# Optimization experiments

Measured on AMD Instinct MI355X. Metric: run time of the kernel, lower is better.

## Reference

```python
import jax, jax.numpy as jnp
import numpy as np

C = 256
NUM_HEADS = 4
GROUPS = 32  # max(1, 256//8), divides 256
EPS = 1e-5


def setup_inputs() -> dict:
    key = jax.random.key(0)
    ks = jax.random.split(key, 7)
    B, H, W = 4, 64, 64
    s = 0.02
    return {
        "x": jax.random.normal(ks[0], (B, C, H, W), dtype=jnp.float32),
        "norm_gamma": jnp.ones((C,), jnp.float32),
        "norm_beta": jnp.zeros((C,), jnp.float32),
        "qkv_w": jax.random.normal(ks[1], (3 * C, C), jnp.float32) * s,  # 1x1 conv kernel squeezed
        "qkv_b": jax.random.normal(ks[2], (3 * C,), jnp.float32) * s,
        "proj_w": jax.random.normal(ks[3], (C, C), jnp.float32) * s,
        "proj_b": jax.random.normal(ks[4], (C,), jnp.float32) * s,
    }


def reference(x, norm_gamma, norm_beta, qkv_w, qkv_b, proj_w, proj_b):
    B, Cc, H, W = x.shape
    hd = Cc // NUM_HEADS
    scale = hd ** -0.5

    # GroupNorm over (channels-per-group, H, W)
    xg = x.reshape(B, GROUPS, Cc // GROUPS, H, W)
    mu = xg.mean(axis=(2, 3, 4), keepdims=True)
    var = xg.var(axis=(2, 3, 4), keepdims=True)
    h = ((xg - mu) * jax.lax.rsqrt(var + EPS)).reshape(B, Cc, H, W)
    h = h * norm_gamma[:, None, None] + norm_beta[:, None, None]

    # 1x1 conv QKV: [B,3C,H,W]
    qkv = jnp.einsum('bchw,oc->bohw', h, qkv_w) + qkv_b[:, None, None]
    q, k, v = jnp.split(qkv, 3, axis=1)

    def heads(t):  # [B,C,H,W] -> [B,nh,HW,hd]
        return t.reshape(B, NUM_HEADS, hd, H * W).transpose(0, 1, 3, 2)

    q, k, v = heads(q), heads(k), heads(v)
    attn = jnp.einsum('bhnd,bhmd->bhnm', q, k) * scale  # [B,nh,HW,HW]
    attn = jax.nn.softmax(attn, axis=-1)
    out = jnp.einsum('bhnm,bhmd->bhnd', attn, v)  # [B,nh,HW,hd]
    out = out.transpose(0, 1, 3, 2).reshape(B, Cc, H, W)

    out = jnp.einsum('bchw,oc->bohw', out, proj_w) + proj_b[:, None, None]
    return x + out
```

## Files before the change

### kernel.cpp

```cpp
#include <hip/hip_runtime.h>
#include <hip/hip_bf16.h>
#include <stdint.h>

typedef unsigned short u16;
typedef __attribute__((ext_vector_type(8))) short bf16x8;
typedef __attribute__((ext_vector_type(4))) float f32x4;
typedef __attribute__((ext_vector_type(16))) float f32x16;

#define HW 4096
#define CC 256
#define QSCALE 0.18033688011112042f

__device__ __forceinline__ u16 f2bf(float f) {
    union { float f; uint32_t i; } v; v.f = f;
    uint32_t x = v.i;
    return (u16)((x + 0x7fffu + ((x >> 16) & 1u)) >> 16);
}

__device__ __forceinline__ float fast_exp2(float x) {
#if __has_builtin(__builtin_amdgcn_exp2f)
    return __builtin_amdgcn_exp2f(x);
#else
    return exp2f(x);
#endif
}

__device__ __forceinline__ unsigned cvt_pk_bf16(float lo, float hi) {
    unsigned r;
    asm("v_cvt_pk_bf16_f32 %0, %1, %2" : "=v"(r) : "v"(lo), "v"(hi));
    return r;
}

__device__ __forceinline__ void plane_swap(unsigned& a, unsigned& b) {
#if __has_builtin(__builtin_amdgcn_permlane32_swap)
    auto r = __builtin_amdgcn_permlane32_swap(a, b, false, false);
    a = r[0]; b = r[1];
#else
    unsigned ax = __shfl_xor((int)a, 32);
    unsigned bx = __shfl_xor((int)b, 32);
    bool hi = (threadIdx.x & 32) != 0;
    unsigned na = hi ? bx : a;
    unsigned nb = hi ? b : ax;
    a = na; b = nb;
#endif
}

#define MFMA16(a, b, c) __builtin_amdgcn_mfma_f32_16x16x32_bf16(a, b, c, 0, 0, 0)
#define MFMA32(a, b, c) __builtin_amdgcn_mfma_f32_32x32x16_bf16(a, b, c, 0, 0, 0)

__global__ void k_wsc(const float* __restrict__ qkv_w, const float* __restrict__ proj_w,
                      const float* __restrict__ x,
                      u16* __restrict__ wqkv, u16* __restrict__ wproj, float* __restrict__ stats) {
    int bid = blockIdx.x;
    if (bid < 1024) {
        int bg = bid >> 3, slab = bid & 7;
        const float4* p = reinterpret_cast<const float4*>(x + (size_t)bg * 32768 + slab * 4096);
        float s = 0.f, ss = 0.f;
        for (int i = 0; i < 4; ++i) {
            float4 v = p[threadIdx.x + i * 256];
            s += v.x + v.y + v.z + v.w;
            ss += v.x * v.x + v.y * v.y + v.z * v.z + v.w * v.w;
        }
        __shared__ float rs[256], rss[256];
        rs[threadIdx.x] = s; rss[threadIdx.x] = ss;
        __syncthreads();
        for (int off = 128; off > 0; off >>= 1) {
            if (threadIdx.x < off) { rs[threadIdx.x] += rs[threadIdx.x + off]; rss[threadIdx.x] += rss[threadIdx.x + off]; }
            __syncthreads();
        }
        if (threadIdx.x == 0) {
            stats[bid * 2] = rs[0];
            stats[bid * 2 + 1] = rss[0];
        }
    } else {
        int i = (bid - 1024) * 256 + threadIdx.x;
        if (i < 768 * 256) {
            int o = i >> 8;
            float sc = (o < 256) ? QSCALE : 1.0f;
            wqkv[i] = f2bf(qkv_w[i] * sc);
        }
        int j = i - 768 * 256;
        if (j >= 0 && j < 256 * 256) wproj[j] = f2bf(proj_w[j]);
    }
}

__global__ __launch_bounds__(256) void k_gnt(const float* __restrict__ x, const float* __restrict__ stats,
                                             const float* __restrict__ gamma, const float* __restrict__ beta,
                                             u16* __restrict__ h_t) {
    int bid = blockIdx.x;
    int b = bid >> 8;
    int cb = (bid >> 6) & 3;
    int nb = bid & 63;
    int t = threadIdx.x;
    int cl = t >> 2;
    int ch = t & 3;
    int c = cb * 64 + cl;
    int g = c >> 3;
    float sum = 0.f, ssum = 0.f;
    for (int s = 0; s < 8; ++s) {
        sum  += stats[((b * 32 + g) * 8 + s) * 2];
        ssum += stats[((b * 32 + g) * 8 + s) * 2 + 1];
    }
    float mu = sum * (1.f / 32768.f);
    float var = ssum * (1.f / 32768.f) - mu * mu;
    float rsg = rsqrtf(var + 1e-5f);
    float ga = gamma[c], be = beta[c];
    __shared__ float T[64][66];
    const float4* p = reinterpret_cast<const float4*>(x + ((size_t)(b * CC + c)) * HW + nb * 64 + ch * 16);
    for (int j = 0; j < 4; ++j) {
        float4 v = p[j];
        int nbase = ch * 16 + j * 4;
        T[nbase + 0][cl] = (v.x - mu) * rsg * ga + be;
        T[nbase + 1][cl] = (v.y - mu) * rsg * ga + be;
        T[nbase + 2][cl] = (v.z - mu) * rsg * ga + be;
        T[nbase + 3][cl] = (v.w - mu) * rsg * ga + be;
    }
    __syncthreads();
    int nl = t >> 2;
    union { u16 u[16]; uint4 q[2]; } pk;
    for (int j = 0; j < 16; ++j) pk.u[j] = f2bf(T[nl][ch * 16 + j]);
    u16* dst = h_t + ((size_t)b * HW + nb * 64 + nl) * CC + cb * 64 + ch * 16;
    *reinterpret_cast<uint4*>(dst) = pk.q[0];
    *reinterpret_cast<uint4*>(dst + 8) = pk.q[1];
}

__global__ __launch_bounds__(256) void k_qkv(const u16* __restrict__ wqkv, const u16* __restrict__ h_t,
                                             const float* __restrict__ qkv_b,
                                             u16* __restrict__ qk_t, u16* __restrict__ v_o) {
    int bid = blockIdx.x;
    int b = bid / 192;
    int rem = bid % 192;
    int om = rem >> 5;
    int nb = rem & 31;
    int o0 = om * 128, n0 = nb * 128;
    int t = threadIdx.x;
    int wid = t >> 6, lane = t & 63;
    int wm = wid >> 1, wn = wid & 1;
    int l15 = lane & 15, lg = lane >> 4;

    __shared__ u16 sA[128 * 40], sB[128 * 40];
    f32x4 acc[4][4];
    for (int i = 0; i < 4; ++i) for (int j = 0; j < 4; ++j) acc[i][j] = (f32x4)0.f;

    const u16* gA = wqkv + (size_t)o0 * 256;
    const u16* gB = h_t + ((size_t)b * HW + n0) * CC;
    int row = t >> 1, half = t & 1;

    for (int kt = 0; kt < 8; ++kt) {
        __syncthreads();
        {
            const uint4* pa = reinterpret_cast<const uint4*>(gA + (size_t)row * 256 + kt * 32 + half * 16);
            uint4 a0 = pa[0], a1 = pa[1];
            const uint4* pb = reinterpret_cast<const uint4*>(gB + (size_t)row * 256 + kt * 32 + half * 16);
            uint4 b0 = pb[0], b1 = pb[1];
            *reinterpret_cast<uint4*>(&sA[row * 40 + half * 16]) = a0;
            *reinterpret_cast<uint4*>(&sA[row * 40 + half * 16 + 8]) = a1;
            *reinterpret_cast<uint4*>(&sB[row * 40 + half * 16]) = b0;
            *reinterpret_cast<uint4*>(&sB[row * 40 + half * 16 + 8]) = b1;
        }
        __syncthreads();
        bf16x8 af[4], bfr[4];
        for (int mt = 0; mt < 4; ++mt)
            af[mt] = *reinterpret_cast<const bf16x8*>(&sA[(wm * 64 + mt * 16 + l15) * 40 + lg * 8]);
        for (int nt = 0; nt < 4; ++nt)
            bfr[nt] = *reinterpret_cast<const bf16x8*>(&sB[(wn * 64 + nt * 16 + l15) * 40 + lg * 8]);
        for (int mt = 0; mt < 4; ++mt)
            for (int nt = 0; nt < 4; ++nt)
                acc[mt][nt] = MFMA16(af[mt], bfr[nt], acc[mt][nt]);
    }

    if (o0 < 512) {
        for (int mt = 0; mt < 4; ++mt) {
            int ob = o0 + wm * 64 + mt * 16 + lg * 4;
            float bias[4];
            for (int r = 0; r < 4; ++r) {
                int o = ob + r;
                bias[r] = qkv_b[o] * (o < 256 ? QSCALE : 1.0f);
            }
            for (int nt = 0; nt < 4; ++nt) {
                int n = n0 + wn * 64 + nt * 16 + l15;
                union { u16 u[4]; uint2 q; } pk;
                for (int r = 0; r < 4; ++r) pk.u[r] = f2bf(acc[mt][nt][r] + bias[r]);
                *reinterpret_cast<uint2*>(qk_t + ((size_t)b * HW + n) * 512 + ob) = pk.q;
            }
        }
    } else {
        for (int mt = 0; mt < 4; ++mt) {
            int ob = o0 + wm * 64 + mt * 16 + lg * 4;
            for (int nt = 0; nt < 4; ++nt) {
                int n = n0 + wn * 64 + nt * 16 + l15;
                for (int r = 0; r < 4; ++r) {
                    int o = ob + r;
                    float bias = qkv_b[o];
                    v_o[((size_t)b * 256 + (o - 512)) * HW + n] = f2bf(acc[mt][nt][r] + bias);
                }
            }
        }
    }
}

__global__ __launch_bounds__(512, 4) void k_attn(const u16* __restrict__ qk_t, const u16* __restrict__ v_o,
                                                 u16* __restrict__ ao_t) {
    int bid = blockIdx.x;
    int swz = (bid & 7) * 64 + (bid >> 3);
    int qb = swz & 31, head = (swz >> 5) & 3, b = swz >> 7;
    int n0 = qb * 128;
    int t = threadIdx.x;
    int kg = t >> 8;
    int wq = (t >> 6) & 3;
    int lane = t & 63, l31 = lane & 31, h = lane >> 5;

    __shared__ u16 lds[2 * 2 * 2 * 64 * 72];

    const u16* qbase = qk_t + ((size_t)b * HW + n0 + wq * 32 + l31) * 512 + head * 64 + h * 8;
    bf16x8 qf[4];
#pragma unroll
    for (int cs = 0; cs < 4; ++cs) qf[cs] = *reinterpret_cast<const bf16x8*>(qbase + cs * 16);

    const u16* gK = qk_t + (size_t)b * HW * 512 + 256 + head * 64;
    const u16* gV = v_o + ((size_t)b * 256 + head * 64) * (size_t)HW;

    int tIn = t & 255;
    int srow = tIn >> 3, sch = tIn & 7;
    const u16* pk0 = gK + (size_t)(kg * 2048 + srow) * 512 + sch * 8;
    const u16* pk1 = pk0 + 32 * 512;
    const u16* pv0 = gV + (size_t)srow * HW + kg * 2048 + sch * 8;
    const u16* pv1 = pv0 + 32 * HW;
    uint4 rk0 = *reinterpret_cast<const uint4*>(pk0);
    uint4 rk1 = *reinterpret_cast<const uint4*>(pk1);
    uint4 rv0 = *reinterpret_cast<const uint4*>(pv0);
    uint4 rv1 = *reinterpret_cast<const uint4*>(pv1);

    f32x16 o0 = (f32x16)0.f, o1 = (f32x16)0.f;
    float l_run = 0.f;
    u16* gb = lds + kg * 18432;

    for (int ti = 0; ti < 32; ++ti) {
        u16* bK = gb + (ti & 1) * 9216;
        u16* bV = bK + 4608;
        *reinterpret_cast<uint4*>(bK + srow * 72 + sch * 8) = rk0;
        *reinterpret_cast<uint4*>(bK + (srow + 32) * 72 + sch * 8) = rk1;
        *reinterpret_cast<uint4*>(bV + srow * 72 + sch * 8) = rv0;
        *reinterpret_cast<uint4*>(bV + (srow + 32) * 72 + sch * 8) = rv1;
        __syncthreads();

        if (ti < 31) {
            pk0 += 64 * 512; pk1 += 64 * 512; pv0 += 64; pv1 += 64;
            rk0 = *reinterpret_cast<const uint4*>(pk0);
            rk1 = *reinterpret_cast<const uint4*>(pk1);
            rv0 = *reinterpret_cast<const uint4*>(pv0);
            rv1 = *reinterpret_cast<const uint4*>(pv1);
        }

        f32x16 s0 = (f32x16)0.f, s1 = (f32x16)0.f;
        __builtin_amdgcn_s_setprio(1);
#pragma unroll
        for (int cs = 0; cs < 4; ++cs) {
            bf16x8 k0 = *reinterpret_cast<const bf16x8*>(bK + l31 * 72 + cs * 16 + h * 8);
            bf16x8 k1 = *reinterpret_cast<const bf16x8*>(bK + (l31 + 32) * 72 + cs * 16 + h * 8);
            s0 = MFMA32(k0, qf[cs], s0);
            s1 = MFMA32(k1, qf[cs], s1);
        }
        __builtin_amdgcn_s_setprio(0);

        float ps = 0.f;
#pragma unroll
        for (int i = 0; i < 16; ++i) { float e = fast_exp2(s0[i]); s0[i] = e; ps += e; }
#pragma unroll
        for (int i = 0; i < 16; ++i) { float e = fast_exp2(s1[i]); s1[i] = e; ps += e; }
        l_run += ps;

        unsigned dws[2][8];
#pragma unroll
        for (int a = 0; a < 4; ++a) {
            dws[0][2 * a]     = cvt_pk_bf16(s0[4 * a],     s0[4 * a + 1]);
            dws[0][2 * a + 1] = cvt_pk_bf16(s0[4 * a + 2], s0[4 * a + 3]);
            dws[1][2 * a]     = cvt_pk_bf16(s1[4 * a],     s1[4 * a + 1]);
            dws[1][2 * a + 1] = cvt_pk_bf16(s1[4 * a + 2], s1[4 * a + 3]);
        }
        bf16x8 pf[4];
#pragma unroll
        for (int ks = 0; ks < 4; ++ks) {
            int kt = ks >> 1, sf = ks & 1;
            unsigned A0 = dws[kt][4 * sf + 0], B0 = dws[kt][4 * sf + 2];
            unsigned A1 = dws[kt][4 * sf + 1], B1 = dws[kt][4 * sf + 3];
            plane_swap(A0, B0);
            plane_swap(A1, B1);
            union { unsigned d[4]; bf16x8 v; } u;
            u.d[0] = A0; u.d[1] = A1; u.d[2] = B0; u.d[3] = B1;
            pf[ks] = u.v;
        }

        __builtin_amdgcn_s_setprio(1);
#pragma unroll
        for (int ks = 0; ks < 4; ++ks) {
            bf16x8 v0 = *reinterpret_cast<const bf16x8*>(bV + l31 * 72 + ks * 16 + h * 8);
            bf16x8 v1 = *reinterpret_cast<const bf16x8*>(bV + (l31 + 32) * 72 + ks * 16 + h * 8);
            o0 = MFMA32(v0, pf[ks], o0);
            o1 = MFMA32(v1, pf[ks], o1);
        }
        __builtin_amdgcn_s_setprio(0);
    }

    l_run += __shfl_xor(l_run, 32);

    float* Of = (float*)lds;
    float* Lf = (float*)lds + 8192;
    u16* E = lds + 18432;

    __syncthreads();
    if (kg == 1) {
#pragma unroll
        for (int i = 0; i < 16; ++i) {
            Of[wq * 2048 + i * 64 + lane] = o0[i];
            Of[wq * 2048 + (16 + i) * 64 + lane] = o1[i];
        }
        Lf[wq * 64 + lane] = l_run;
    }
    __syncthreads();
    if (kg == 0) {
#pragma unroll
        for (int i = 0; i < 16; ++i) {
            o0[i] += Of[wq * 2048 + i * 64 + lane];
            o1[i] += Of[wq * 2048 + (16 + i) * 64 + lane];
        }
        l_run += Lf[wq * 64 + lane];
        float inv = 1.0f / l_run;
        int qrow = wq * 32 + l31;
#pragma unroll
        for (int r = 0; r < 16; ++r) {
            int d = (r & 3) + 8 * (r >> 2) + 4 * h;
            E[qrow * 72 + d]      = f2bf(o0[r] * inv);
            E[qrow * 72 + 32 + d] = f2bf(o1[r] * inv);
        }
    }
    __syncthreads();
#pragma unroll
    for (int i = 0; i < 2; ++i) {
        int item = i * 512 + t;
        int row = item >> 3, cb = item & 7;
        uint4 w = *reinterpret_cast<const uint4*>(E + row * 72 + cb * 8);
        *reinterpret_cast<uint4*>(ao_t + ((size_t)b * HW + n0 + row) * 256 + head * 64 + cb * 8) = w;
    }
}

__global__ __launch_bounds__(256) void k_proj(const u16* __restrict__ wproj, const u16* __restrict__ ao_t,
                                              const float* __restrict__ proj_b, const float* __restrict__ x,
                                              float* __restrict__ out) {
    int bid = blockIdx.x;
    int b = bid >> 7;
    int om = (bid >> 6) & 1;
    int nb = bid & 63;
    int o0 = om * 128, n0 = nb * 64;
    int t = threadIdx.x;
    int wid = t >> 6, lane = t & 63;
    int wm = wid >> 1, wn = wid & 1;
    int l15 = lane & 15, lg = lane >> 4;

    __shared__ u16 sA[128 * 40], sB[64 * 40];
    f32x4 acc[4][2];
    for (int i = 0; i < 4; ++i) for (int j = 0; j < 2; ++j) acc[i][j] = (f32x4)0.f;

    const u16* gA = wproj + (size_t)o0 * 256;
    const u16* gB = ao_t + ((size_t)b * HW + n0) * CC;
    int rowA = t >> 1, halfA = t & 1;
    int rowB = t >> 2, qB = t & 3;

    for (int kt = 0; kt < 8; ++kt) {
        __syncthreads();
        {
            const uint4* pa = reinterpret_cast<const uint4*>(gA + (size_t)rowA * 256 + kt * 32 + halfA * 16);
            uint4 a0 = pa[0], a1 = pa[1];
            uint4 b0 = *reinterpret_cast<const uint4*>(gB + (size_t)rowB * 256 + kt * 32 + qB * 8);
            *reinterpret_cast<uint4*>(&sA[rowA * 40 + halfA * 16]) = a0;
            *reinterpret_cast<uint4*>(&sA[rowA * 40 + halfA * 16 + 8]) = a1;
            *reinterpret_cast<uint4*>(&sB[rowB * 40 + qB * 8]) = b0;
        }
        __syncthreads();
        bf16x8 af[4], bfr[2];
        for (int mt = 0; mt < 4; ++mt)
            af[mt] = *reinterpret_cast<const bf16x8*>(&sA[(wm * 64 + mt * 16 + l15) * 40 + lg * 8]);
        for (int nt = 0; nt < 2; ++nt)
            bfr[nt] = *reinterpret_cast<const bf16x8*>(&sB[(wn * 32 + nt * 16 + l15) * 40 + lg * 8]);
        for (int mt = 0; mt < 4; ++mt)
            for (int nt = 0; nt < 2; ++nt)
                acc[mt][nt] = MFMA16(af[mt], bfr[nt], acc[mt][nt]);
    }

    for (int mt = 0; mt < 4; ++mt) {
        int ob = o0 + wm * 64 + mt * 16 + lg * 4;
        for (int nt = 0; nt < 2; ++nt) {
            int n = n0 + wn * 32 + nt * 16 + l15;
            for (int r = 0; r < 4; ++r) {
                int o = ob + r;
                size_t idx = ((size_t)(b * CC + o)) * HW + n;
                out[idx] = acc[mt][nt][r] + proj_b[o] + x[idx];
            }
        }
    }
}

extern "C" void kernel_launch(void* const* d_in, const int* in_sizes, int n_in,
                              void* d_out, int out_size, void* d_ws, size_t ws_size,
                              hipStream_t stream) {
    const float* x      = (const float*)d_in[0];
    const float* gamma  = (const float*)d_in[1];
    const float* beta   = (const float*)d_in[2];
    const float* qkv_w  = (const float*)d_in[3];
    const float* qkv_b  = (const float*)d_in[4];
    const float* proj_w = (const float*)d_in[5];
    const float* proj_b = (const float*)d_in[6];
    float* out = (float*)d_out;
    char* ws = (char*)d_ws;

    float* stats = (float*)ws;
    u16* wqkv  = (u16*)(ws + 8192);
    u16* wproj = (u16*)(ws + 8192 + 393216);
    u16* h_t   = (u16*)(ws + 1048576);
    u16* qk_t  = (u16*)(ws + 1048576 + 8388608);
    u16* v_o   = (u16*)(ws + 1048576 + 8388608 + 16777216);
    u16* ao_t  = (u16*)(ws + 1048576 + 8388608 + 16777216 + 8388608);

    k_wsc<<<dim3(2048), dim3(256), 0, stream>>>(qkv_w, proj_w, x, wqkv, wproj, stats);
    k_gnt<<<dim3(1024), dim3(256), 0, stream>>>(x, stats, gamma, beta, h_t);
    k_qkv<<<dim3(768), dim3(256), 0, stream>>>(wqkv, h_t, qkv_b, qk_t, v_o);
    k_attn<<<dim3(512), dim3(512), 0, stream>>>(qk_t, v_o, ao_t);
    k_proj<<<dim3(512), dim3(256), 0, stream>>>(wproj, ao_t, proj_b, x, out);
}
```

Before: 122.8 us.

## Fuse GroupNorm-normalize-transpose into QKV GEMM, staging normalized activations in LDS

```diff
diff --git a/kernel.cpp b/kernel.cpp
--- a/kernel.cpp
+++ b/kernel.cpp
@@ -84,49 +84,11 @@
     }
 }
 
-__global__ __launch_bounds__(256) void k_gnt(const float* __restrict__ x, const float* __restrict__ stats,
-                                             const float* __restrict__ gamma, const float* __restrict__ beta,
-                                             u16* __restrict__ h_t) {
-    int bid = blockIdx.x;
-    int b = bid >> 8;
-    int cb = (bid >> 6) & 3;
-    int nb = bid & 63;
-    int t = threadIdx.x;
-    int cl = t >> 2;
-    int ch = t & 3;
-    int c = cb * 64 + cl;
-    int g = c >> 3;
-    float sum = 0.f, ssum = 0.f;
-    for (int s = 0; s < 8; ++s) {
-        sum  += stats[((b * 32 + g) * 8 + s) * 2];
-        ssum += stats[((b * 32 + g) * 8 + s) * 2 + 1];
-    }
-    float mu = sum * (1.f / 32768.f);
-    float var = ssum * (1.f / 32768.f) - mu * mu;
-    float rsg = rsqrtf(var + 1e-5f);
-    float ga = gamma[c], be = beta[c];
-    __shared__ float T[64][66];
-    const float4* p = reinterpret_cast<const float4*>(x + ((size_t)(b * CC + c)) * HW + nb * 64 + ch * 16);
-    for (int j = 0; j < 4; ++j) {
-        float4 v = p[j];
-        int nbase = ch * 16 + j * 4;
-        T[nbase + 0][cl] = (v.x - mu) * rsg * ga + be;
-        T[nbase + 1][cl] = (v.y - mu) * rsg * ga + be;
-        T[nbase + 2][cl] = (v.z - mu) * rsg * ga + be;
-        T[nbase + 3][cl] = (v.w - mu) * rsg * ga + be;
-    }
-    __syncthreads();
-    int nl = t >> 2;
-    union { u16 u[16]; uint4 q[2]; } pk;
-    for (int j = 0; j < 16; ++j) pk.u[j] = f2bf(T[nl][ch * 16 + j]);
-    u16* dst = h_t + ((size_t)b * HW + nb * 64 + nl) * CC + cb * 64 + ch * 16;
-    *reinterpret_cast<uint4*>(dst) = pk.q[0];
-    *reinterpret_cast<uint4*>(dst + 8) = pk.q[1];
-}
-
-__global__ __launch_bounds__(256) void k_qkv(const u16* __restrict__ wqkv, const u16* __restrict__ h_t,
-                                             const float* __restrict__ qkv_b,
-                                             u16* __restrict__ qk_t, u16* __restrict__ v_o) {
+__global__ __launch_bounds__(256) void k_qkvf(const u16* __restrict__ wqkv, const float* __restrict__ x,
+                                              const float* __restrict__ stats,
+                                              const float* __restrict__ gamma, const float* __restrict__ beta,
+                                              const float* __restrict__ qkv_b,
+                                              u16* __restrict__ qk_t, u16* __restrict__ v_o) {
     int bid = blockIdx.x;
     int b = bid / 192;
     int rem = bid % 192;
@@ -138,12 +100,53 @@
     int wm = wid >> 1, wn = wid & 1;
     int l15 = lane & 15, lg = lane >> 4;
 
-    __shared__ u16 sA[128 * 40], sB[128 * 40];
+    __shared__ u16 sA[128 * 40];
+    __shared__ u16 hB[128 * 264];
+
+    {
+        int cpair = t >> 1;
+        int nh = t & 1;
+        int c0 = cpair * 2;
+        float mu[2], rsg[2], ga[2], be[2];
+#pragma unroll
+        for (int e = 0; e < 2; ++e) {
+            int c = c0 + e;
+            int g = c >> 3;
+            float sum = 0.f, ssum = 0.f;
+            for (int s = 0; s < 8; ++s) {
+                sum  += stats[((b * 32 + g) * 8 + s) * 2];
+                ssum += stats[((b * 32 + g) * 8 + s) * 2 + 1];
+            }
+            float m = sum * (1.f / 32768.f);
+            float var = ssum * (1.f / 32768.f) - m * m;
+            mu[e] = m;
+            rsg[e] = rsqrtf(var + 1e-5f);
+            ga[e] = gamma[c];
+            be[e] = beta[c];
+        }
+        const float4* px0 = reinterpret_cast<const float4*>(x + ((size_t)(b * CC + c0)) * HW + n0 + nh * 64);
+        const float4* px1 = reinterpret_cast<const float4*>(x + ((size_t)(b * CC + c0 + 1)) * HW + n0 + nh * 64);
+#pragma unroll
+        for (int j4 = 0; j4 < 16; ++j4) {
+            float4 v0 = px0[j4];
+            float4 v1 = px1[j4];
+            float a0[4] = {v0.x, v0.y, v0.z, v0.w};
+            float a1[4] = {v1.x, v1.y, v1.z, v1.w};
+#pragma unroll
+            for (int k = 0; k < 4; ++k) {
+                u16 lo = f2bf((a0[k] - mu[0]) * rsg[0] * ga[0] + be[0]);
+                u16 hi = f2bf((a1[k] - mu[1]) * rsg[1] * ga[1] + be[1]);
+                unsigned pk = (unsigned)lo | ((unsigned)hi << 16);
+                *reinterpret_cast<unsigned*>(&hB[(nh * 64 + j4 * 4 + k) * 264 + c0]) = pk;
+            }
+        }
+    }
+    __syncthreads();
+
     f32x4 acc[4][4];
     for (int i = 0; i < 4; ++i) for (int j = 0; j < 4; ++j) acc[i][j] = (f32x4)0.f;
 
     const u16* gA = wqkv + (size_t)o0 * 256;
-    const u16* gB = h_t + ((size_t)b * HW + n0) * CC;
     int row = t >> 1, half = t & 1;
 
     for (int kt = 0; kt < 8; ++kt) {
@@ -151,19 +154,15 @@
         {
             const uint4* pa = reinterpret_cast<const uint4*>(gA + (size_t)row * 256 + kt * 32 + half * 16);
             uint4 a0 = pa[0], a1 = pa[1];
-            const uint4* pb = reinterpret_cast<const uint4*>(gB + (size_t)row * 256 + kt * 32 + half * 16);
-            uint4 b0 = pb[0], b1 = pb[1];
             *reinterpret_cast<uint4*>(&sA[row * 40 + half * 16]) = a0;
             *reinterpret_cast<uint4*>(&sA[row * 40 + half * 16 + 8]) = a1;
-            *reinterpret_cast<uint4*>(&sB[row * 40 + half * 16]) = b0;
-            *reinterpret_cast<uint4*>(&sB[row * 40 + half * 16 + 8]) = b1;
         }
         __syncthreads();
         bf16x8 af[4], bfr[4];
         for (int mt = 0; mt < 4; ++mt)
             af[mt] = *reinterpret_cast<const bf16x8*>(&sA[(wm * 64 + mt * 16 + l15) * 40 + lg * 8]);
         for (int nt = 0; nt < 4; ++nt)
-            bfr[nt] = *reinterpret_cast<const bf16x8*>(&sB[(wn * 64 + nt * 16 + l15) * 40 + lg * 8]);
+            bfr[nt] = *reinterpret_cast<const bf16x8*>(&hB[(wn * 64 + nt * 16 + l15) * 264 + kt * 32 + lg * 8]);
         for (int mt = 0; mt < 4; ++mt)
             for (int nt = 0; nt < 4; ++nt)
                 acc[mt][nt] = MFMA16(af[mt], bfr[nt], acc[mt][nt]);
@@ -416,14 +415,12 @@
     float* stats = (float*)ws;
     u16* wqkv  = (u16*)(ws + 8192);
     u16* wproj = (u16*)(ws + 8192 + 393216);
-    u16* h_t   = (u16*)(ws + 1048576);
-    u16* qk_t  = (u16*)(ws + 1048576 + 8388608);
-    u16* v_o   = (u16*)(ws + 1048576 + 8388608 + 16777216);
-    u16* ao_t  = (u16*)(ws + 1048576 + 8388608 + 16777216 + 8388608);
+    u16* qk_t  = (u16*)(ws + 1048576);
+    u16* v_o   = (u16*)(ws + 1048576 + 16777216);
+    u16* ao_t  = (u16*)(ws + 1048576 + 16777216 + 8388608);
 
     k_wsc<<<dim3(2048), dim3(256), 0, stream>>>(qkv_w, proj_w, x, wqkv, wproj, stats);
-    k_gnt<<<dim3(1024), dim3(256), 0, stream>>>(x, stats, gamma, beta, h_t);
-    k_qkv<<<dim3(768), dim3(256), 0, stream>>>(wqkv, h_t, qkv_b, qk_t, v_o);
+    k_qkvf<<<dim3(768), dim3(256), 0, stream>>>(wqkv, x, stats, gamma, beta, qkv_b, qk_t, v_o);
     k_attn<<<dim3(512), dim3(512), 0, stream>>>(qk_t, v_o, ao_t);
     k_proj<<<dim3(512), dim3(256), 0, stream>>>(wproj, ao_t, proj_b, x, out);
 }
```

Result: slower. 128.0 us (+4.2%).
